# Kernel optimization log

Hardware: AMD Instinct MI355X
Metric: run time of the kernel (lower is better)

## Reference

```python
import jax, jax.numpy as jnp
import numpy as np

IN_FEATURES = 4096
OUT_FEATURES = 11008
B, S = 8, 512


def setup_inputs() -> dict:
    key = jax.random.key(0)
    k1, k2, k3 = jax.random.split(key, 3)
    x = jax.random.normal(k1, (B, S, IN_FEATURES), dtype=jnp.float32)
    # int8 weights simulated as int32 values in [-127, 127]
    weight_int8 = jax.random.randint(k2, (OUT_FEATURES, IN_FEATURES), -127, 128, dtype=jnp.int32)
    # per-output-channel scales (positive, small, like absmax/127)
    weight_scale = jax.random.uniform(k3, (OUT_FEATURES,), dtype=jnp.float32) * 0.01 + 1e-4
    return {"x": x, "weight_int8": weight_int8, "weight_scale": weight_scale}


def reference(x, weight_int8, weight_scale):
    # On-the-fly dequantization: W[o, i] = int8[o, i] * scale[o]
    weight = weight_int8.astype(x.dtype) * weight_scale.astype(x.dtype)[:, None]
    # F.linear: y = x @ W^T  -> [B, S, out_features]
    return jnp.einsum('bsi,oi->bso', x, weight)
```

## Files before the change

kernel.cpp:

```cpp
#include <hip/hip_runtime.h>
#include <hip/hip_bf16.h>
#include <stdint.h>

#define M_DIM 4096
#define N_DIM 11008
#define K_DIM 4096

typedef int   i32x4 __attribute__((ext_vector_type(4)));

static __device__ __forceinline__ void direct_load16(const void* gptr, void* ldsptr) {
    __builtin_amdgcn_global_load_lds(
        (const __attribute__((address_space(1))) void*)gptr,
        (__attribute__((address_space(3))) void*)ldsptr,
        16, 0, 0);
}

__global__ __launch_bounds__(256) void cvt_w_kernel(const int* __restrict__ w,
                                                    int8_t* __restrict__ o) {
    int t = blockIdx.x * 256 + threadIdx.x;
    const int4* w4 = (const int4*)w;
    int4 a = w4[2 * t];
    int4 b = w4[2 * t + 1];
    uint2 r;
    r.x = (a.x & 255) | ((a.y & 255) << 8) | ((a.z & 255) << 16) | (a.w << 24);
    r.y = (b.x & 255) | ((b.y & 255) << 8) | ((b.z & 255) << 16) | (b.w << 24);
    ((uint2*)o)[t] = r;
}

__global__ __launch_bounds__(256) void quant_x_kernel(const float* __restrict__ x,
                                                      int8_t* __restrict__ xq,
                                                      float* __restrict__ xs) {
    __shared__ float wmax[4];
    const int row = blockIdx.x;
    const int t = threadIdx.x;
    const float4* xr = (const float4*)(x + (size_t)row * K_DIM);

    float4 v[4];
    float am = 0.0f;
#pragma unroll
    for (int p = 0; p < 4; p++) {
        v[p] = xr[p * 256 + t];
        am = fmaxf(am, fmaxf(fmaxf(fabsf(v[p].x), fabsf(v[p].y)),
                             fmaxf(fabsf(v[p].z), fabsf(v[p].w))));
    }
#pragma unroll
    for (int o = 32; o > 0; o >>= 1)
        am = fmaxf(am, __shfl_xor(am, o));
    if ((t & 63) == 0) wmax[t >> 6] = am;
    __syncthreads();
    am = fmaxf(fmaxf(wmax[0], wmax[1]), fmaxf(wmax[2], wmax[3]));

    const float inv = 127.0f / am;
    int* oq = (int*)(xq + (size_t)row * K_DIM);
#pragma unroll
    for (int p = 0; p < 4; p++) {
        int qa = (int)rintf(v[p].x * inv);
        int qb = (int)rintf(v[p].y * inv);
        int qc = (int)rintf(v[p].z * inv);
        int qd = (int)rintf(v[p].w * inv);
        oq[p * 256 + t] = (qa & 255) | ((qb & 255) << 8) | ((qc & 255) << 16) | (qd << 24);
    }
    if (t == 0) xs[row] = am * (1.0f / 127.0f);
}


__global__ __launch_bounds__(256) void gemm_i8_kernel(
    const int8_t* __restrict__ A,
    const int8_t* __restrict__ B,
    const float* __restrict__ xs,
    const float* __restrict__ ws,
    float* __restrict__ C)
{
    __shared__ int8_t As[128 * 64];
    __shared__ int8_t Bs[128 * 64];

    const int tid  = threadIdx.x;
    const int lane = tid & 63;
    const int wave = tid >> 6;
    const int wm   = wave >> 1;
    const int wn   = wave & 1;
    const int quad = lane >> 4;
    const int r16  = lane & 15;

    const int m0 = blockIdx.x * 128;
    const int n0 = blockIdx.y * 128;

    const int lrow = tid >> 2;
    const int lcol = (tid & 3) * 16;
    const int8_t* ga0 = A + (size_t)(m0 + lrow) * K_DIM + lcol;
    const int8_t* ga1 = A + (size_t)(m0 + 64 + lrow) * K_DIM + lcol;
    const int8_t* gb0 = B + (size_t)(n0 + lrow) * K_DIM + lcol;
    const int8_t* gb1 = B + (size_t)(n0 + 64 + lrow) * K_DIM + lcol;

    char* lAs = (char*)As;
    char* lBs = (char*)Bs;
    const int wb = wave * 1024;

    i32x4 acc[4][4];
#pragma unroll
    for (int i = 0; i < 4; i++)
#pragma unroll
        for (int j = 0; j < 4; j++) acc[i][j] = (i32x4)(0);

    for (int k0 = 0; k0 < K_DIM; k0 += 64) {
        direct_load16(ga0, lAs + wb);
        direct_load16(ga1, lAs + 4096 + wb);
        direct_load16(gb0, lBs + wb);
        direct_load16(gb1, lBs + 4096 + wb);
        ga0 += 64; ga1 += 64; gb0 += 64; gb1 += 64;
        __syncthreads();

        i32x4 af[4], bf[4];
#pragma unroll
        for (int i = 0; i < 4; i++)
            af[i] = *(const i32x4*)&As[(wm * 64 + i * 16 + r16) * 64 + quad * 16];
#pragma unroll
        for (int j = 0; j < 4; j++)
            bf[j] = *(const i32x4*)&Bs[(wn * 64 + j * 16 + r16) * 64 + quad * 16];

#pragma unroll
        for (int i = 0; i < 4; i++)
#pragma unroll
            for (int j = 0; j < 4; j++)
                acc[i][j] = __builtin_amdgcn_mfma_i32_16x16x64_i8(af[i], bf[j], acc[i][j], 0, 0, 0);

        __syncthreads();
    }

    float rs[4][4];
#pragma unroll
    for (int i = 0; i < 4; i++) {
        const int mrow = m0 + wm * 64 + i * 16 + quad * 4;
#pragma unroll
        for (int r = 0; r < 4; r++) rs[i][r] = xs[mrow + r];
    }
#pragma unroll
    for (int j = 0; j < 4; j++) {
        const int n = n0 + wn * 64 + j * 16 + r16;
        const float s = ws[n];
#pragma unroll
        for (int i = 0; i < 4; i++) {
            const int mrow = m0 + wm * 64 + i * 16 + quad * 4;
#pragma unroll
            for (int r = 0; r < 4; r++)
                C[(size_t)(mrow + r) * N_DIM + n] = (float)acc[i][j][r] * s * rs[i][r];
        }
    }
}


extern "C" void kernel_launch(void* const* d_in, const int* in_sizes, int n_in,
                              void* d_out, int out_size, void* d_ws, size_t ws_size,
                              hipStream_t stream) {
    const float* x       = (const float*)d_in[0];
    const int*   w_int   = (const int*)d_in[1];
    const float* w_scale = (const float*)d_in[2];
    float*       out     = (float*)d_out;

    int8_t* wq = (int8_t*)d_ws;
    int8_t* xq = (int8_t*)((char*)d_ws + (size_t)N_DIM * K_DIM);
    float*  xs = (float*)((char*)d_ws + (size_t)N_DIM * K_DIM + (size_t)M_DIM * K_DIM);

    cvt_w_kernel<<<dim3(22016), dim3(256), 0, stream>>>(w_int, wq);
    quant_x_kernel<<<dim3(M_DIM), dim3(256), 0, stream>>>(x, xq, xs);
    gemm_i8_kernel<<<dim3(M_DIM / 128, N_DIM / 128), dim3(256), 0, stream>>>(xq, wq, xs, w_scale, out);
}
```

Measured before the change: 619.3 us.

## Double K-tile to 128 and XOR-swizzle LDS layout for int8 GEMM

Each main-loop iteration of the int8 GEMM now covers 128 K elements instead of 64, which halves the number of barrier pairs per tile. Each thread loads a 16-byte chunk whose column is XOR-swizzled by its row, and the fragment reads apply the same swizzle to avoid LDS bank conflicts on the 128-byte row stride. LDS use rises to 32 KB per block, which may lower occupancy, and there is still no double buffering.

Result: faster. 588.6 us (-5.0%).

```diff
diff --git a/kernel.cpp b/kernel.cpp
--- a/kernel.cpp
+++ b/kernel.cpp
@@ -6,7 +6,7 @@
 #define N_DIM 11008
 #define K_DIM 4096
 
-typedef int   i32x4 __attribute__((ext_vector_type(4)));
+typedef int i32x4 __attribute__((ext_vector_type(4)));
 
 static __device__ __forceinline__ void direct_load16(const void* gptr, void* ldsptr) {
     __builtin_amdgcn_global_load_lds(
@@ -71,8 +71,8 @@
     const float* __restrict__ ws,
     float* __restrict__ C)
 {
-    __shared__ int8_t As[128 * 64];
-    __shared__ int8_t Bs[128 * 64];
+    __shared__ __align__(16) int8_t As[128 * 128];
+    __shared__ __align__(16) int8_t Bs[128 * 128];
 
     const int tid  = threadIdx.x;
     const int lane = tid & 63;
@@ -81,16 +81,15 @@
     const int wn   = wave & 1;
     const int quad = lane >> 4;
     const int r16  = lane & 15;
+    const int sw   = r16 & 7;
 
     const int m0 = blockIdx.x * 128;
     const int n0 = blockIdx.y * 128;
 
-    const int lrow = tid >> 2;
-    const int lcol = (tid & 3) * 16;
-    const int8_t* ga0 = A + (size_t)(m0 + lrow) * K_DIM + lcol;
-    const int8_t* ga1 = A + (size_t)(m0 + 64 + lrow) * K_DIM + lcol;
-    const int8_t* gb0 = B + (size_t)(n0 + lrow) * K_DIM + lcol;
-    const int8_t* gb1 = B + (size_t)(n0 + 64 + lrow) * K_DIM + lcol;
+    const int srow = tid >> 3;
+    const int scol = ((tid & 7) ^ (srow & 7)) * 16;
+    const int8_t* gA = A + (size_t)(m0 + srow) * K_DIM + scol;
+    const int8_t* gB = B + (size_t)(n0 + srow) * K_DIM + scol;
 
     char* lAs = (char*)As;
     char* lBs = (char*)Bs;
@@ -102,27 +101,34 @@
 #pragma unroll
         for (int j = 0; j < 4; j++) acc[i][j] = (i32x4)(0);
 
-    for (int k0 = 0; k0 < K_DIM; k0 += 64) {
-        direct_load16(ga0, lAs + wb);
-        direct_load16(ga1, lAs + 4096 + wb);
-        direct_load16(gb0, lBs + wb);
-        direct_load16(gb1, lBs + 4096 + wb);
-        ga0 += 64; ga1 += 64; gb0 += 64; gb1 += 64;
+    for (int k0 = 0; k0 < K_DIM; k0 += 128) {
+#pragma unroll
+        for (int p = 0; p < 4; p++) {
+            direct_load16(gA + (size_t)(p * 32) * K_DIM, lAs + p * 4096 + wb);
+            direct_load16(gB + (size_t)(p * 32) * K_DIM, lBs + p * 4096 + wb);
+        }
+        gA += 128; gB += 128;
         __syncthreads();
 
-        i32x4 af[4], bf[4];
 #pragma unroll
-        for (int i = 0; i < 4; i++)
-            af[i] = *(const i32x4*)&As[(wm * 64 + i * 16 + r16) * 64 + quad * 16];
+        for (int s = 0; s < 2; s++) {
+            i32x4 af[4], bf[4];
 #pragma unroll
-        for (int j = 0; j < 4; j++)
-            bf[j] = *(const i32x4*)&Bs[(wn * 64 + j * 16 + r16) * 64 + quad * 16];
-
+            for (int i = 0; i < 4; i++) {
+                const int arow = wm * 64 + i * 16 + r16;
+                af[i] = *(const i32x4*)&As[arow * 128 + ((s * 4 + quad) ^ sw) * 16];
+            }
 #pragma unroll
-        for (int i = 0; i < 4; i++)
+            for (int j = 0; j < 4; j++) {
+                const int brow = wn * 64 + j * 16 + r16;
+                bf[j] = *(const i32x4*)&Bs[brow * 128 + ((s * 4 + quad) ^ sw) * 16];
+            }
 #pragma unroll
-            for (int j = 0; j < 4; j++)
-                acc[i][j] = __builtin_amdgcn_mfma_i32_16x16x64_i8(af[i], bf[j], acc[i][j], 0, 0, 0);
+            for (int i = 0; i < 4; i++)
+#pragma unroll
+                for (int j = 0; j < 4; j++)
+                    acc[i][j] = __builtin_amdgcn_mfma_i32_16x16x64_i8(af[i], bf[j], acc[i][j], 0, 0, 0);
+        }
 
         __syncthreads();
     }
```
